# Optimization experiments

Hardware: AMD Instinct MI355X
Metric: run time of the kernel (lower is better)

## Reference

```python
import jax, jax.numpy as jnp
import numpy as np

N = 100_000
D_FEAT = 64
HALF_DEG = 8              # node v connects to v+-o (mod N), o=1..8 -> degree 16
K = 2 * HALF_DEG + 1      # neighborhood incl. self
KNN = 4                   # DifferentiableEmbeddingUTS(k_neighbors=4)
EPS = 1e-12


def setup_inputs() -> dict:
    key = jax.random.key(0)
    kx, k1, k2 = jax.random.split(key, 3)
    x = jax.random.normal(kx, (N, D_FEAT), dtype=jnp.float32)

    offs = np.arange(1, HALF_DEG + 1)
    src = np.repeat(np.arange(N), HALF_DEG)
    dst = (src + np.tile(offs, N)) % N
    edge_index = jnp.asarray(np.stack([src, dst]).astype(np.int64))  # (2, 800k)

    # padded fixed-size neighborhoods: {v} U {v+-o} -- exactly what the
    # original dict/loop builds (set([v]+nbrs[v])), here uniform size K
    all_offs = np.concatenate([[0], offs, -offs])
    nbr_idx = (np.arange(N)[:, None] + all_offs[None, :]) % N
    nbr_idx = jnp.asarray(nbr_idx.astype(np.int64))                  # (N, K)

    W1 = jax.random.normal(k1, (7, 64), dtype=jnp.float32) * 0.1
    b1 = jnp.zeros((64,), dtype=jnp.float32)
    W2 = jax.random.normal(k2, (64, 1), dtype=jnp.float32) * 0.1
    b2 = jnp.zeros((1,), dtype=jnp.float32)
    return {"x": x, "edge_index": edge_index, "nbr_idx": nbr_idx,
            "W1": W1, "b1": b1, "W2": W2, "b2": b2}


def _uts_stats(H):
    """H: (N, K, d) neighborhood embeddings -> (N, 7) differentiable UTS vector.
    Stats: [mean, std, max, min] of centroid distances, mean/std of pairwise
    distances, mean k-NN distance (k=KNN)."""
    n, k, _ = H.shape
    c = H.mean(axis=1, keepdims=True)                         # centroid
    dc = jnp.sqrt(jnp.sum((H - c) ** 2, axis=-1) + EPS)        # (N, K)
    f_mean, f_std = dc.mean(1), dc.std(1)
    f_max, f_min = dc.max(1), dc.min(1)

    sq = jnp.sum(H * H, axis=-1)                               # (N, K)
    D2 = sq[:, :, None] + sq[:, None, :] - 2.0 * jnp.einsum('nkd,nld->nkl', H, H)
    D = jnp.sqrt(jnp.clip(D2, 0.0) + EPS)                      # (N, K, K)

    n_off = k * (k - 1)                                        # off-diagonal count
    pw_mean = D.sum(axis=(1, 2)) / n_off
    pw_m2 = (D * D).sum(axis=(1, 2)) / n_off
    pw_std = jnp.sqrt(jnp.clip(pw_m2 - pw_mean ** 2, 0.0) + EPS)

    Ds = jnp.sort(D, axis=-1)                                  # col 0 is self (=~0)
    knn_mean = Ds[:, :, 1:KNN + 1].mean(axis=(1, 2))

    return jnp.stack([f_mean, f_std, f_max, f_min, pw_mean, pw_std, knn_mean], axis=-1)


def reference(x, edge_index, nbr_idx, W1, b1, W2, b2):
    # edge_index is subsumed by the precomputed padded nbr_idx (same graph).
    H = x[nbr_idx]                     # (N, K, d) ragged gather, padded uniform
    uts = _uts_stats(H)                # (N, 7)
    h = jax.nn.relu(uts @ W1 + b1)     # (N, 64)
    scores = (h @ W2 + b2)[:, 0]       # (N,)
    return scores
```

## Files before the change

### kernel.cpp

```cpp
#include <hip/hip_runtime.h>
#include <math.h>

#define NN     100000
#define K      17
#define HALF   8
#define VB     64
#define GRID   ((NN + VB - 1) / VB)
#define NROWS  80
#define BS     20
#define FTSZ   1581
#define EPSF   1e-12f
#define BIGF   3e38f

typedef _Float16 half2v __attribute__((ext_vector_type(2)));
typedef _Float16 half8v __attribute__((ext_vector_type(8)));

#if defined(__has_builtin)
#if __has_builtin(__builtin_amdgcn_fdot2)
#define HAVE_FDOT2 1
#endif
#endif

__device__ __forceinline__ float fdot2f(half2v a, half2v b, float c) {
#ifdef HAVE_FDOT2
    return __builtin_amdgcn_fdot2(a, b, c, false);
#else
    return fmaf((float)a.x, (float)b.x, fmaf((float)a.y, (float)b.y, c));
#endif
}

union H8 { half8v v; half2v p[4]; };


__global__ __launch_bounds__(256, 7) void uts_score_kernel(
    const float* __restrict__ x,
    const float* __restrict__ W1,
    const float* __restrict__ b1,
    const float* __restrict__ W2,
    const float* __restrict__ b2,
    float* __restrict__ out)
{
    __shared__ _Float16 hrows[NROWS * 64];
    __shared__ float    sqs[NROWS];
    __shared__ float2   ftab[FTSZ];

    const int tid = threadIdx.x;
    const int v0  = blockIdx.x * VB;

    #pragma unroll
    for (int k = 0; k < 3; ++k) {
        const int idx = tid + 256 * k;
        const bool act = idx < NROWS * 8;
        float ps = 0.f;
        int r = 0, s = 0;
        if (act) {
            r = idx >> 3;
            s = idx & 7;
            int gr = v0 - HALF + r;
            if (gr < 0)   gr += NN;
            if (gr >= NN) gr -= NN;
            const float* src = x + (size_t)gr * 64 + s * 8;
            const float4 f0 = *reinterpret_cast<const float4*>(src);
            const float4 f1 = *reinterpret_cast<const float4*>(src + 4);
            H8 h;
            h.v = (half8v){(_Float16)f0.x, (_Float16)f0.y, (_Float16)f0.z, (_Float16)f0.w,
                           (_Float16)f1.x, (_Float16)f1.y, (_Float16)f1.z, (_Float16)f1.w};
            const int slot = s ^ (r & 7);
            *reinterpret_cast<half8v*>(&hrows[r * 64 + (slot << 3)]) = h.v;
            ps = fdot2f(h.p[0], h.p[0], 0.f);
            ps = fdot2f(h.p[1], h.p[1], ps);
            ps = fdot2f(h.p[2], h.p[2], ps);
            ps = fdot2f(h.p[3], h.p[3], ps);
        }
        ps += __shfl_xor(ps, 1);
        ps += __shfl_xor(ps, 2);
        ps += __shfl_xor(ps, 4);
        if (act && s == 0) sqs[r] = ps;
    }
    __syncthreads();

    if (tid < 240) {
        const int base = tid % 80;
        const int part = tid / 80;
        const int d0   = part * 6;
        const int nd   = (part == 2) ? 5 : 6;
        float acc[6] = {0.f, 0.f, 0.f, 0.f, 0.f, 0.f};
        const int bmask = base & 7;
        #pragma unroll
        for (int sc = 0; sc < 8; ++sc) {
            H8 a;
            a.v = *reinterpret_cast<const half8v*>(&hrows[base * 64 + ((sc ^ bmask) << 3)]);
            #pragma unroll
            for (int dd = 0; dd < 6; ++dd) {
                const int nr = base + d0 + dd;
                if (dd < nd && nr < NROWS) {
                    H8 c;
                    c.v = *reinterpret_cast<const half8v*>(&hrows[nr * 64 + ((sc ^ (nr & 7)) << 3)]);
                    float s = acc[dd];
                    s = fdot2f(a.p[0], c.p[0], s);
                    s = fdot2f(a.p[1], c.p[1], s);
                    s = fdot2f(a.p[2], c.p[2], s);
                    s = fdot2f(a.p[3], c.p[3], s);
                    acc[dd] = s;
                }
            }
        }
        const float sqa = sqs[base];
        #pragma unroll
        for (int dd = 0; dd < 6; ++dd) {
            const int d  = d0 + dd;
            const int nr = base + d;
            if (dd < nd && nr < NROWS) {
                const float g = acc[dd];
                const float d2 = (d == 0) ? 0.f
                                          : fmaxf(fmaf(-2.f, g, sqa + sqs[nr]), 0.f);
                float2 e;
                e.x = g;
                e.y = sqrtf(d2 + EPSF);
                ftab[base * BS + d] = e;
            }
        }
    }
    __syncthreads();

    const int nl = tid >> 2;
    const int t  = tid & 3;
    const int v  = v0 + nl;
    const float2* win2 = ftab + nl * BS;

    float sqv[5];
    float psq = 0.f;
    #pragma unroll
    for (int r = 0; r < 5; ++r) {
        const int i = t + 4 * r;
        if (i < K) { sqv[r] = sqs[nl + i]; psq += sqv[r]; }
        else       { sqv[r] = 0.f; }
    }

    float prs = 0.f, pD = 0.f, pknn = 0.f;
    float rsv[5];

    #pragma unroll
    for (int r = 0; r < 5; ++r) {
        const int i = t + 4 * r;
        rsv[r] = 0.f;
        if (i < K) {
            float rs = 0.f, rowD = 0.f;
            float k0 = BIGF, k1 = BIGF, k2 = BIGF, k3 = BIGF;
            #pragma unroll
            for (int j = 0; j < K; ++j) {
                const int m   = (j < i) ? j : i;
                const int off = 18 * m + i + j;
                const float2 e = win2[off];
                rs   += e.x;
                rowD += e.y;
                const float cand = (j == i) ? BIGF : e.y;
                const float M0 = fmaxf(k0, cand); k0 = fminf(k0, cand);
                const float M1 = fmaxf(k1, M0);   k1 = fminf(k1, M0);
                const float M2 = fmaxf(k2, M1);   k2 = fminf(k2, M1);
                k3 = fminf(k3, M2);
            }
            rsv[r] = rs;
            prs  += rs;
            pD   += rowD;
            pknn += (k0 + k1) + (k2 + k3);
        }
    }

    psq  += __shfl_xor(psq,  1); psq  += __shfl_xor(psq,  2);
    prs  += __shfl_xor(prs,  1); prs  += __shfl_xor(prs,  2);
    pD   += __shfl_xor(pD,   1); pD   += __shfl_xor(pD,   2);
    pknn += __shfl_xor(pknn, 1); pknn += __shfl_xor(pknn, 2);
    const float sqsum = psq;

    const float pD2 = fmaf(34.f, sqsum, -2.f * prs) + 2.89e-10f;

    const float csq = prs * (1.f / 289.f);
    float dcv[5];
    float dsum = 0.f, dmax = -BIGF, dmin = BIGF;
    #pragma unroll
    for (int r = 0; r < 5; ++r) {
        const int i = t + 4 * r;
        if (i < K) {
            float val = sqv[r] - 2.f * rsv[r] * (1.f / 17.f) + csq + EPSF;
            val = fmaxf(val, 0.f);
            const float dc = sqrtf(val);
            dcv[r] = dc;
            dsum += dc;
            dmax = fmaxf(dmax, dc);
            dmin = fminf(dmin, dc);
        } else {
            dcv[r] = 0.f;
        }
    }
    dsum += __shfl_xor(dsum, 1); dsum += __shfl_xor(dsum, 2);
    dmax = fmaxf(dmax, __shfl_xor(dmax, 1)); dmax = fmaxf(dmax, __shfl_xor(dmax, 2));
    dmin = fminf(dmin, __shfl_xor(dmin, 1)); dmin = fminf(dmin, __shfl_xor(dmin, 2));

    const float f_mean = dsum * (1.f / 17.f);
    float vsum = 0.f;
    #pragma unroll
    for (int r = 0; r < 5; ++r) {
        const int i = t + 4 * r;
        if (i < K) {
            const float d = dcv[r] - f_mean;
            vsum = fmaf(d, d, vsum);
        }
    }
    vsum += __shfl_xor(vsum, 1); vsum += __shfl_xor(vsum, 2);
    const float f_std = sqrtf(vsum * (1.f / 17.f));

    const float pw_mean = pD * (1.f / 272.f);
    const float pw_m2   = pD2 * (1.f / 272.f);
    const float pw_var  = fmaxf(pw_m2 - pw_mean * pw_mean, 0.f);
    const float pw_std  = sqrtf(pw_var + EPSF);
    const float knn_mean = pknn * (1.f / 68.f);

    float uts[7];
    uts[0] = f_mean;
    uts[1] = f_std;
    uts[2] = dmax;
    uts[3] = dmin;
    uts[4] = pw_mean;
    uts[5] = pw_std;
    uts[6] = knn_mean;

    float h[16];
    {
        const float4* b1v = reinterpret_cast<const float4*>(b1 + t * 16);
        #pragma unroll
        for (int q = 0; q < 4; ++q) {
            const float4 bb = b1v[q];
            h[q * 4 + 0] = bb.x; h[q * 4 + 1] = bb.y;
            h[q * 4 + 2] = bb.z; h[q * 4 + 3] = bb.w;
        }
    }
    #pragma unroll
    for (int f = 0; f < 7; ++f) {
        const float uf = uts[f];
        const float4* wrow = reinterpret_cast<const float4*>(W1 + f * 64 + t * 16);
        #pragma unroll
        for (int q = 0; q < 4; ++q) {
            const float4 w = wrow[q];
            h[q * 4 + 0] = fmaf(uf, w.x, h[q * 4 + 0]);
            h[q * 4 + 1] = fmaf(uf, w.y, h[q * 4 + 1]);
            h[q * 4 + 2] = fmaf(uf, w.z, h[q * 4 + 2]);
            h[q * 4 + 3] = fmaf(uf, w.w, h[q * 4 + 3]);
        }
    }
    float score = 0.f;
    {
        const float4* w2v = reinterpret_cast<const float4*>(W2 + t * 16);
        #pragma unroll
        for (int q = 0; q < 4; ++q) {
            const float4 w = w2v[q];
            score = fmaf(fmaxf(h[q * 4 + 0], 0.f), w.x, score);
            score = fmaf(fmaxf(h[q * 4 + 1], 0.f), w.y, score);
            score = fmaf(fmaxf(h[q * 4 + 2], 0.f), w.z, score);
            score = fmaf(fmaxf(h[q * 4 + 3], 0.f), w.w, score);
        }
    }
    score += __shfl_xor(score, 1);
    score += __shfl_xor(score, 2);

    if (t == 0 && v < NN) out[v] = score + b2[0];
}

extern "C" void kernel_launch(void* const* d_in, const int* in_sizes, int n_in,
                              void* d_out, int out_size, void* d_ws, size_t ws_size,
                              hipStream_t stream) {
    const float* x  = (const float*)d_in[0];
    const float* W1 = (const float*)d_in[3];
    const float* b1 = (const float*)d_in[4];
    const float* W2 = (const float*)d_in[5];
    const float* b2 = (const float*)d_in[6];
    float* out = (float*)d_out;

    hipLaunchKernelGGL(uts_score_kernel, dim3(GRID), dim3(256), 0, stream,
                       x, W1, b1, W2, b2, out);
}
```

Baseline: 33.24 us.

## Compute banded Gram matrix with MFMA 16x16x32 f16 tiles instead of fdot2

Replaces the per-thread fdot2 band dot-products with wave-level MFMA 16x16x32 f16 tiles over diagonal and super-diagonal 16-row blocks. Only the 17-wide band is written to a raw staging buffer, and squared norms are taken from its diagonal. A separate pass then converts the band into the distance table. Shared memory is aliased so the fp16 rows and the distance table share space, and the launch-bounds occupancy hint is raised. This trades extra MFMA work on unused off-band entries and an additional barrier for fewer scalar dot instructions.

```diff
diff --git a/kernel.cpp b/kernel.cpp
--- a/kernel.cpp
+++ b/kernel.cpp
@@ -7,32 +7,18 @@
 #define VB     64
 #define GRID   ((NN + VB - 1) / VB)
 #define NROWS  80
+#define GS     17
+#define GRSZ   (NROWS * GS)
 #define BS     20
 #define FTSZ   1581
 #define EPSF   1e-12f
 #define BIGF   3e38f
 
-typedef _Float16 half2v __attribute__((ext_vector_type(2)));
 typedef _Float16 half8v __attribute__((ext_vector_type(8)));
-
-#if defined(__has_builtin)
-#if __has_builtin(__builtin_amdgcn_fdot2)
-#define HAVE_FDOT2 1
-#endif
-#endif
-
-__device__ __forceinline__ float fdot2f(half2v a, half2v b, float c) {
-#ifdef HAVE_FDOT2
-    return __builtin_amdgcn_fdot2(a, b, c, false);
-#else
-    return fmaf((float)a.x, (float)b.x, fmaf((float)a.y, (float)b.y, c));
-#endif
-}
-
-union H8 { half8v v; half2v p[4]; };
-
-
-__global__ __launch_bounds__(256, 7) void uts_score_kernel(
+typedef float    f32x4  __attribute__((ext_vector_type(4)));
+
+
+__global__ __launch_bounds__(256, 8) void uts_score_kernel(
     const float* __restrict__ x,
     const float* __restrict__ W1,
     const float* __restrict__ b1,
@@ -40,9 +26,11 @@
     const float* __restrict__ b2,
     float* __restrict__ out)
 {
-    __shared__ _Float16 hrows[NROWS * 64];
-    __shared__ float    sqs[NROWS];
-    __shared__ float2   ftab[FTSZ];
+    __shared__ __align__(16) unsigned char smem[12648 + 5440 + 320];
+    _Float16* hrows = reinterpret_cast<_Float16*>(smem);
+    float2*   ftab  = reinterpret_cast<float2*>(smem);
+    float*    graw  = reinterpret_cast<float*>(smem + 12648);
+    float*    sqs   = reinterpret_cast<float*>(smem + 12648 + 5440);
 
     const int tid = threadIdx.x;
     const int v0  = blockIdx.x * VB;
@@ -50,74 +38,76 @@
     #pragma unroll
     for (int k = 0; k < 3; ++k) {
         const int idx = tid + 256 * k;
-        const bool act = idx < NROWS * 8;
-        float ps = 0.f;
-        int r = 0, s = 0;
-        if (act) {
-            r = idx >> 3;
-            s = idx & 7;
+        if (idx < NROWS * 8) {
+            const int r = idx >> 3;
+            const int s = idx & 7;
             int gr = v0 - HALF + r;
             if (gr < 0)   gr += NN;
             if (gr >= NN) gr -= NN;
             const float* src = x + (size_t)gr * 64 + s * 8;
             const float4 f0 = *reinterpret_cast<const float4*>(src);
             const float4 f1 = *reinterpret_cast<const float4*>(src + 4);
-            H8 h;
-            h.v = (half8v){(_Float16)f0.x, (_Float16)f0.y, (_Float16)f0.z, (_Float16)f0.w,
-                           (_Float16)f1.x, (_Float16)f1.y, (_Float16)f1.z, (_Float16)f1.w};
-            const int slot = s ^ (r & 7);
-            *reinterpret_cast<half8v*>(&hrows[r * 64 + (slot << 3)]) = h.v;
-            ps = fdot2f(h.p[0], h.p[0], 0.f);
-            ps = fdot2f(h.p[1], h.p[1], ps);
-            ps = fdot2f(h.p[2], h.p[2], ps);
-            ps = fdot2f(h.p[3], h.p[3], ps);
-        }
-        ps += __shfl_xor(ps, 1);
-        ps += __shfl_xor(ps, 2);
-        ps += __shfl_xor(ps, 4);
-        if (act && s == 0) sqs[r] = ps;
+            half8v h = {(_Float16)f0.x, (_Float16)f0.y, (_Float16)f0.z, (_Float16)f0.w,
+                        (_Float16)f1.x, (_Float16)f1.y, (_Float16)f1.z, (_Float16)f1.w};
+            *reinterpret_cast<half8v*>(&hrows[r * 64 + ((s ^ (r & 7)) << 3)]) = h;
+        }
     }
     __syncthreads();
 
-    if (tid < 240) {
-        const int base = tid % 80;
-        const int part = tid / 80;
-        const int d0   = part * 6;
-        const int nd   = (part == 2) ? 5 : 6;
-        float acc[6] = {0.f, 0.f, 0.f, 0.f, 0.f, 0.f};
-        const int bmask = base & 7;
-        #pragma unroll
-        for (int sc = 0; sc < 8; ++sc) {
-            H8 a;
-            a.v = *reinterpret_cast<const half8v*>(&hrows[base * 64 + ((sc ^ bmask) << 3)]);
+    {
+        const int wid = tid >> 6;
+        const int l   = tid & 63;
+        const int lr  = l & 15;
+        const int kb  = l >> 4;
+        #pragma unroll 1
+        for (int tp = wid; tp < 9; tp += 4) {
+            const int ti = (tp < 5) ? tp : (tp - 5);
+            const int tj = (tp < 5) ? tp : (tp - 4);
+            const int ra = ti * 16 + lr;
+            const int rb = tj * 16 + lr;
+            const half8v a0 = *reinterpret_cast<const half8v*>(
+                &hrows[ra * 64 + (((kb    ) ^ (ra & 7)) << 3)]);
+            const half8v a1 = *reinterpret_cast<const half8v*>(
+                &hrows[ra * 64 + (((kb + 4) ^ (ra & 7)) << 3)]);
+            half8v b0, b1;
+            if (ti == tj) { b0 = a0; b1 = a1; }
+            else {
+                b0 = *reinterpret_cast<const half8v*>(
+                    &hrows[rb * 64 + (((kb    ) ^ (rb & 7)) << 3)]);
+                b1 = *reinterpret_cast<const half8v*>(
+                    &hrows[rb * 64 + (((kb + 4) ^ (rb & 7)) << 3)]);
+            }
+            f32x4 c = {0.f, 0.f, 0.f, 0.f};
+            c = __builtin_amdgcn_mfma_f32_16x16x32_f16(a0, b0, c, 0, 0, 0);
+            c = __builtin_amdgcn_mfma_f32_16x16x32_f16(a1, b1, c, 0, 0, 0);
+            const int bcol = tj * 16 + lr;
             #pragma unroll
-            for (int dd = 0; dd < 6; ++dd) {
-                const int nr = base + d0 + dd;
-                if (dd < nd && nr < NROWS) {
-                    H8 c;
-                    c.v = *reinterpret_cast<const half8v*>(&hrows[nr * 64 + ((sc ^ (nr & 7)) << 3)]);
-                    float s = acc[dd];
-                    s = fdot2f(a.p[0], c.p[0], s);
-                    s = fdot2f(a.p[1], c.p[1], s);
-                    s = fdot2f(a.p[2], c.p[2], s);
-                    s = fdot2f(a.p[3], c.p[3], s);
-                    acc[dd] = s;
+            for (int r = 0; r < 4; ++r) {
+                const int arow = ti * 16 + kb * 4 + r;
+                const int d    = bcol - arow;
+                if (d >= 0 && d <= 16) {
+                    graw[arow * GS + d] = c[r];
+                    if (d == 0) sqs[arow] = c[r];
                 }
             }
         }
-        const float sqa = sqs[base];
-        #pragma unroll
-        for (int dd = 0; dd < 6; ++dd) {
-            const int d  = d0 + dd;
-            const int nr = base + d;
-            if (dd < nd && nr < NROWS) {
-                const float g = acc[dd];
+    }
+    __syncthreads();
+
+    #pragma unroll
+    for (int k = 0; k < 6; ++k) {
+        const int idx = tid + 256 * k;
+        if (idx < GRSZ) {
+            const int b = idx / GS;
+            const int d = idx - b * GS;
+            if (b + d < NROWS) {
+                const float g  = graw[idx];
                 const float d2 = (d == 0) ? 0.f
-                                          : fmaxf(fmaf(-2.f, g, sqa + sqs[nr]), 0.f);
+                                          : fmaxf(fmaf(-2.f, g, sqs[b] + sqs[b + d]), 0.f);
                 float2 e;
                 e.x = g;
                 e.y = sqrtf(d2 + EPSF);
-                ftab[base * BS + d] = e;
+                ftab[b * BS + d] = e;
             }
         }
     }
```

After: 32.96 us. No clear change (-0.9%).
